# Kernel tuning notes

Hardware: AMD Instinct MI355X
Metric: run time of the kernel (lower is better)

Reference implementation:

```python
import jax, jax.numpy as jnp
import numpy as np

B, T, NH, MD, FF, HEADS, OUT, PEH = 8, 4096, 16, 64, 256, 4, 1, 32
DH = MD // HEADS

def _ln(x, g, b, eps=1e-5):
    m = jnp.mean(x, -1, keepdims=True)
    v = jnp.mean((x - m) ** 2, -1, keepdims=True)
    return (x - m) * jax.lax.rsqrt(v + eps) * g + b

def _lrelu(x):
    return jax.nn.leaky_relu(x, 0.2)

def setup_inputs():
    key = jax.random.key(0)
    ks = jax.random.split(key, 16)
    w = lambda k, s: jax.random.normal(k, s, jnp.float32) * 0.02
    return dict(
        x=jax.random.normal(ks[0], (B, T, MD), jnp.float32),
        coords1=jax.random.uniform(ks[1], (T,), jnp.float32),
        coords2=jax.random.uniform(ks[2], (T,), jnp.float32),
        g1=jnp.ones((MD,), jnp.float32), be1=jnp.zeros((MD,), jnp.float32),
        Wq=w(ks[3], (MD, MD)), bq=jnp.zeros((MD,), jnp.float32),
        Wk=w(ks[4], (MD, MD)), bk=jnp.zeros((MD,), jnp.float32),
        Wv=w(ks[5], (MD, MD)), bv=jnp.zeros((MD,), jnp.float32),
        logit_scale=jnp.full((HEADS, 1, 1), jnp.log(10.0), jnp.float32),
        Wo=w(ks[6], (MD, MD)), bo=jnp.zeros((MD,), jnp.float32),
        Wp1=w(ks[7], (2, PEH)), bp1=jnp.zeros((PEH,), jnp.float32),
        Wp2=w(ks[8], (PEH, HEADS)), bp2=jnp.zeros((HEADS,), jnp.float32),
        g2=jnp.ones((MD,), jnp.float32), be2=jnp.zeros((MD,), jnp.float32),
        Wn1=w(ks[9], (MD, FF)), bn1=jnp.zeros((FF,), jnp.float32),
        Wn2=w(ks[10], (FF, 1)), bn2=jnp.zeros((1,), jnp.float32),
        g3=jnp.ones((MD * NH,), jnp.float32), be3=jnp.zeros((MD * NH,), jnp.float32),
        Wu1=w(ks[11], (MD * NH, MD * NH)), bu1=jnp.zeros((MD * NH,), jnp.float32),
        Wu2=w(ks[12], (MD * NH, OUT)), bu2=jnp.zeros((OUT,), jnp.float32),
    )

def reference(x, coords1, coords2, g1, be1, Wq, bq, Wk, bk, Wv, bv, logit_scale, Wo, bo,
              Wp1, bp1, Wp2, bp2, g2, be2, Wn1, bn1, Wn2, bn2, g3, be3, Wu1, bu1, Wu2, bu2):
    b, t, e = x.shape
    xn = _ln(x, g1, be1)
    # pairwise relative coords: d[i, j] = c[j] - c[i]  -> [t, t]
    d1 = coords1[None, :] - coords1[:, None]
    d2 = coords2[None, :] - coords2[:, None]
    _, idx = jax.lax.top_k(-(d1 * d1 + d2 * d2), NH)          # [t, nh] kNN indices (incl. self)
    xg = xn[:, idx, :]                                         # [b, t, nh, e] neighbor gather
    c1 = jnp.take_along_axis(d1, idx, axis=1)                  # [t, nh] rel coords of neighbors
    c2 = jnp.take_along_axis(d2, idx, axis=1)
    # relative-position bias among the nh neighbors (shared across batch)
    p = jnp.stack([c1[:, :, None] - c1[:, None, :],
                   c2[:, :, None] - c2[:, None, :]], -1)       # [t, nh, nh, 2]
    bias = _lrelu(p @ Wp1 + bp1) @ Wp2 + bp2                   # [t, nh, nh, H]
    bias = jnp.transpose(bias, (0, 3, 1, 2))                   # [t, H, nh, nh]
    xf = xg.reshape(b * t, NH, e)
    split = lambda z: jnp.transpose(z.reshape(b * t, NH, HEADS, DH), (0, 2, 1, 3))
    qh = split(xf @ Wq + bq)
    kh = split(xf @ Wk + bk)
    vh = split(xf @ Wv + bv)
    # cosine attention with learnable clamped logit scale (SwinV2-style)
    qh = qh / jnp.maximum(jnp.linalg.norm(qh, axis=-1, keepdims=True), 1e-6)
    kh = kh / jnp.maximum(jnp.linalg.norm(kh, axis=-1, keepdims=True), 1e-6)
    scale = jnp.exp(jnp.minimum(logit_scale, jnp.log(100.0)))  # [H,1,1]
    att = jnp.einsum('nhqd,nhkd->nhqk', qh, kh) * scale        # [b*t, H, nh, nh]
    att = att.reshape(b, t, HEADS, NH, NH) + bias[None]
    att = jax.nn.softmax(att, -1).reshape(b * t, HEADS, NH, NH)
    av = jnp.einsum('nhqk,nhkd->nhqd', att, vh)
    av = jnp.transpose(av, (0, 2, 1, 3)).reshape(b * t, NH, e)
    xf = xf + (av @ Wo + bo)                                   # residual 1 (dropout=0)
    xf = _ln(xf, g2, be2)
    xf = xf + _lrelu(_lrelu(xf @ Wn1 + bn1) @ Wn2 + bn2)       # residual 2, [.,.,1] broadcast
    xu = _ln(xf.reshape(b, t, NH * e), g3, be3)                # unfold neighbors
    return _lrelu(_lrelu(xu @ Wu1 + bu1) @ Wu2 + bu2)          # [b, t, OUT]
```

## Files before the change

kernel.cpp:

```cpp
#include <hip/hip_runtime.h>
#include <hip/hip_bf16.h>

#define BB 8
#define TT 4096
#define NHH 16
#define MDD 64
#define FFF 256
#define HEADSS 4
#define DHH 16
#define PEHH 32

#define GM (BB * TT)
#define GK 1024
#define GN 1024
#define BMt 128
#define BNt 128
#define BKt 64
#define NCHUNK (GN / BNt)

#define TOKW 4

typedef float f32x4 __attribute__((ext_vector_type(4)));
typedef short bf16x8 __attribute__((ext_vector_type(8)));

static __device__ __forceinline__ float lrelu(float x) { return x > 0.0f ? x : 0.2f * x; }
static __device__ __forceinline__ unsigned long long umin64(unsigned long long a, unsigned long long b) {
    return a < b ? a : b;
}
static __device__ __forceinline__ unsigned short f2bf(float f) {
    unsigned u = __float_as_uint(f);
    u = u + 0x7fffu + ((u >> 16) & 1u);
    return (unsigned short)(u >> 16);
}
static __device__ __forceinline__ float bf2f(unsigned short u) {
    return __uint_as_float(((unsigned)u) << 16);
}
static __device__ __forceinline__ unsigned pk2(float a, float b) {
    return (unsigned)f2bf(a) | ((unsigned)f2bf(b) << 16);
}
static __device__ __forceinline__ void gload16(const void* g, void* l) {
    __builtin_amdgcn_global_load_lds((const __attribute__((address_space(1))) unsigned int*)g,
                                     (__attribute__((address_space(3))) unsigned int*)l, 16, 0, 0);
}

__global__ __launch_bounds__(256) void k_neighbors(const float* __restrict__ c1,
                                                   const float* __restrict__ c2,
                                                   int* __restrict__ idx,
                                                   float* __restrict__ c1n,
                                                   float* __restrict__ c2n) {
    int t = blockIdx.x;
    int tid = threadIdx.x;
    int lane = tid & 63, w = tid >> 6;
    __shared__ unsigned long long stage[4 * NHH];
    float c1t = c1[t], c2t = c2[t];

    unsigned long long keys[16];
    #pragma unroll
    for (int i = 0; i < 16; ++i) {
        int j = i * 256 + tid;
        float d1 = __fsub_rn(c1[j], c1t);
        float d2 = __fsub_rn(c2[j], c2t);
        float dist = __fadd_rn(__fmul_rn(d1, d1), __fmul_rn(d2, d2));
        keys[i] = (((unsigned long long)__float_as_uint(dist)) << 32) | (unsigned)j;
    }

    #pragma unroll 1
    for (int s = 0; s < NHH; ++s) {
        unsigned long long m = keys[0];
        #pragma unroll
        for (int i = 1; i < 16; ++i) m = umin64(m, keys[i]);
        #pragma unroll
        for (int off = 1; off < 64; off <<= 1)
            m = umin64(m, (unsigned long long)__shfl_xor((long long)m, off));
        #pragma unroll
        for (int i = 0; i < 16; ++i)
            if (keys[i] == m) keys[i] = ~0ull;
        if (lane == 0) stage[w * NHH + s] = m;
    }
    __syncthreads();

    if (w == 0) {
        unsigned long long k0 = stage[lane];
        #pragma unroll 1
        for (int s = 0; s < NHH; ++s) {
            unsigned long long m = k0;
            #pragma unroll
            for (int off = 1; off < 64; off <<= 1)
                m = umin64(m, (unsigned long long)__shfl_xor((long long)m, off));
            if (k0 == m) k0 = ~0ull;
            if (lane == 0) {
                int jj = (int)(unsigned)(m & 0xffffffffu);
                idx[t * NHH + s] = jj;
                c1n[t * NHH + s] = __fsub_rn(c1[jj], c1t);
                c2n[t * NHH + s] = __fsub_rn(c2[jj], c2t);
            }
        }
    }
}

__global__ __launch_bounds__(256) void k_bias(const float* __restrict__ c1n,
                                              const float* __restrict__ c2n,
                                              const float* __restrict__ Wp1,
                                              const float* __restrict__ bp1,
                                              const float* __restrict__ Wp2,
                                              const float* __restrict__ bp2,
                                              float* __restrict__ bias) {
    __shared__ float sWp1[2 * PEHH], sbp1[PEHH], sWp2[PEHH * HEADSS], sbp2[HEADSS];
    int tid = threadIdx.x;
    if (tid < 2 * PEHH) sWp1[tid] = Wp1[tid];
    if (tid < PEHH) sbp1[tid] = bp1[tid];
    if (tid < PEHH * HEADSS) sWp2[tid] = Wp2[tid];
    if (tid < HEADSS) sbp2[tid] = bp2[tid];
    __syncthreads();
    int g = blockIdx.x * 256 + tid;
    if (g >= TT * NHH * NHH) return;
    int j = g & 15, i = (g >> 4) & 15, t = g >> 8;
    float p1 = c1n[t * NHH + i] - c1n[t * NHH + j];
    float p2 = c2n[t * NHH + i] - c2n[t * NHH + j];
    float acc0 = sbp2[0], acc1 = sbp2[1], acc2 = sbp2[2], acc3 = sbp2[3];
    #pragma unroll
    for (int kk = 0; kk < PEHH; ++kk) {
        float h = lrelu(p1 * sWp1[kk] + p2 * sWp1[PEHH + kk] + sbp1[kk]);
        acc0 += h * sWp2[kk * HEADSS + 0];
        acc1 += h * sWp2[kk * HEADSS + 1];
        acc2 += h * sWp2[kk * HEADSS + 2];
        acc3 += h * sWp2[kk * HEADSS + 3];
    }
    float* bt = bias + (size_t)t * HEADSS * NHH * NHH;
    bt[(0 * NHH + i) * NHH + j] = acc0;
    bt[(1 * NHH + i) * NHH + j] = acc1;
    bt[(2 * NHH + i) * NHH + j] = acc2;
    bt[(3 * NHH + i) * NHH + j] = acc3;
}

__global__ __launch_bounds__(256) void k_ln1(const float* __restrict__ x,
                                             const float* __restrict__ g1,
                                             const float* __restrict__ be1,
                                             unsigned short* __restrict__ xn) {
    int row = blockIdx.x * 4 + (threadIdx.x >> 6);
    int lane = threadIdx.x & 63;
    float v = x[(size_t)row * MDD + lane];
    float s = v;
    for (int off = 32; off > 0; off >>= 1) s += __shfl_down(s, off);
    s = __shfl(s, 0);
    float m = s * (1.0f / 64.0f);
    float d = v - m;
    float sq = d * d;
    for (int off = 32; off > 0; off >>= 1) sq += __shfl_down(sq, off);
    sq = __shfl(sq, 0);
    float var = sq * (1.0f / 64.0f);
    float inv = 1.0f / sqrtf(var + 1e-5f);
    xn[(size_t)row * MDD + lane] = f2bf(d * inv * g1[lane] + be1[lane]);
}

__global__ __launch_bounds__(256) void k_prepw(const float* __restrict__ Wq, const float* __restrict__ Wk,
                                               const float* __restrict__ Wv, const float* __restrict__ Wo,
                                               const float* __restrict__ Wn1,
                                               unsigned short* __restrict__ Wall) {
    int id = blockIdx.x * 256 + threadIdx.x;
    int f = id >> 9;
    int w = (id >> 3) & 63;
    int e = id & 7;
    int li = w & 15, G = w >> 4;
    float v;
    if (f < 24) {
        int mt = f >> 1, ks = f & 1;
        int n = mt * 16 + li;
        int k = ks * 32 + G * 8 + e;
        v = (n < 64) ? Wq[k * 64 + n] : (n < 128) ? Wk[k * 64 + (n - 64)] : Wv[k * 64 + (n - 128)];
    } else if (f < 32) {
        int g2i = f - 24;
        int mt = g2i >> 1, ks = g2i & 1;
        int n = mt * 16 + li;
        int k = ks * 32 + G * 8 + e;
        v = Wo[k * 64 + n];
    } else {
        int g2i = f - 32;
        int mt = g2i >> 1, ks = g2i & 1;
        int n = mt * 16 + li;
        int k = ks * 32 + G * 8 + e;
        v = Wn1[k * 256 + n];
    }
    Wall[id] = f2bf(v);
}

__global__ __launch_bounds__(256, 4) void k_main(const unsigned short* __restrict__ xnb,
                                              const int* __restrict__ idx,
                                              const float* __restrict__ bias,
                                              const unsigned short* __restrict__ Wall,
                                              const float* __restrict__ bq, const float* __restrict__ bk,
                                              const float* __restrict__ bv, const float* __restrict__ ls,
                                              const float* __restrict__ bo,
                                              const float* __restrict__ g2, const float* __restrict__ be2,
                                              const float* __restrict__ bn1, const float* __restrict__ Wn2,
                                              const float* __restrict__ bn2,
                                              const float* __restrict__ g3, const float* __restrict__ be3,
                                              unsigned short* __restrict__ xu) {
    __shared__ __align__(16) char L[TOKW * 9216];
    const int tid = threadIdx.x;
    const int lane = tid & 63;
    const int li = lane & 15;
    const int G = lane >> 4;
    const int tok = tid >> 6;
    const int nglob = blockIdx.x * TOKW + tok;
    const int b = nglob >> 12;
    const int t = nglob & (TT - 1);
    const int asw = (li & 7) << 4;

    char* xgT = L + tok * 9216;
    char* qT  = xgT + 2048;
    char* kT  = xgT + 4096;
    char* vT  = xgT + 6144;

    {
        int r16 = lane >> 2, part = lane & 3;
        int j = idx[t * NHH + r16];
        const uint4* sp = reinterpret_cast<const uint4*>(xnb + ((size_t)b * TT + j) * MDD + part * 16);
        uint4 w0 = sp[0], w1 = sp[1];
        int sw = (r16 & 7) << 4;
        *reinterpret_cast<uint4*>(xgT + r16 * 128 + ((part * 32) ^ sw)) = w0;
        *reinterpret_cast<uint4*>(xgT + r16 * 128 + ((part * 32 + 16) ^ sw)) = w1;
    }

    bf16x8 xf0 = *reinterpret_cast<const bf16x8*>(xgT + li * 128 + ((G * 16) ^ asw));
    bf16x8 xf1 = *reinterpret_cast<const bf16x8*>(xgT + li * 128 + ((64 + G * 16) ^ asw));
    f32x4 acc[12];
    #pragma unroll
    for (int mt = 0; mt < 12; ++mt) {
        bf16x8 w0 = *reinterpret_cast<const bf16x8*>(Wall + (mt * 2 + 0) * 512 + lane * 8);
        bf16x8 w1 = *reinterpret_cast<const bf16x8*>(Wall + (mt * 2 + 1) * 512 + lane * 8);
        f32x4 a = (f32x4){0.0f, 0.0f, 0.0f, 0.0f};
        a = __builtin_amdgcn_mfma_f32_16x16x32_bf16(w0, xf0, a, 0, 0, 0);
        a = __builtin_amdgcn_mfma_f32_16x16x32_bf16(w1, xf1, a, 0, 0, 0);
        acc[mt] = a;
    }
    #pragma unroll
    for (int h = 0; h < 4; ++h) {
        float4 b4 = *reinterpret_cast<const float4*>(bq + h * 16 + G * 4);
        float q0 = acc[h][0] + b4.x, q1 = acc[h][1] + b4.y, q2 = acc[h][2] + b4.z, q3 = acc[h][3] + b4.w;
        float sq = q0 * q0 + q1 * q1 + q2 * q2 + q3 * q3;
        sq += __shfl_xor(sq, 16); sq += __shfl_xor(sq, 32);
        float iq = 1.0f / fmaxf(sqrtf(sq), 1e-6f);
        uint2 u; u.x = pk2(q0 * iq, q1 * iq); u.y = pk2(q2 * iq, q3 * iq);
        *reinterpret_cast<uint2*>(qT + li * 128 + ((h * 32 + G * 8) ^ asw)) = u;
    }
    #pragma unroll
    for (int h = 0; h < 4; ++h) {
        float4 b4 = *reinterpret_cast<const float4*>(bk + h * 16 + G * 4);
        float k0 = acc[4 + h][0] + b4.x, k1 = acc[4 + h][1] + b4.y, k2 = acc[4 + h][2] + b4.z, k3 = acc[4 + h][3] + b4.w;
        float sk = k0 * k0 + k1 * k1 + k2 * k2 + k3 * k3;
        sk += __shfl_xor(sk, 16); sk += __shfl_xor(sk, 32);
        float ik = 1.0f / fmaxf(sqrtf(sk), 1e-6f);
        uint2 u; u.x = pk2(k0 * ik, k1 * ik); u.y = pk2(k2 * ik, k3 * ik);
        *reinterpret_cast<uint2*>(kT + li * 128 + ((h * 32 + G * 8) ^ asw)) = u;
    }
    #pragma unroll
    for (int m2 = 0; m2 < 4; ++m2) {
        float4 b4 = *reinterpret_cast<const float4*>(bv + m2 * 16 + G * 4);
        float v0 = acc[8 + m2][0] + b4.x, v1 = acc[8 + m2][1] + b4.y, v2 = acc[8 + m2][2] + b4.z, v3 = acc[8 + m2][3] + b4.w;
        int c0 = m2 * 16 + G * 4;
        *reinterpret_cast<unsigned short*>(vT + (c0 + 0) * 48 + li * 2) = f2bf(v0);
        *reinterpret_cast<unsigned short*>(vT + (c0 + 1) * 48 + li * 2) = f2bf(v1);
        *reinterpret_cast<unsigned short*>(vT + (c0 + 2) * 48 + li * 2) = f2bf(v2);
        *reinterpret_cast<unsigned short*>(vT + (c0 + 3) * 48 + li * 2) = f2bf(v3);
    }

    float lsa[4] = {ls[0], ls[1], ls[2], ls[3]};

    #pragma unroll
    for (int h = 0; h < 4; ++h) {
        bf16x8 kf8 = {}, qf8 = {};
        if (G < 2) {
            kf8 = *reinterpret_cast<const bf16x8*>(kT + li * 128 + ((h * 32 + G * 16) ^ asw));
            qf8 = *reinterpret_cast<const bf16x8*>(qT + li * 128 + ((h * 32 + G * 16) ^ asw));
        }
        f32x4 s4 = __builtin_amdgcn_mfma_f32_16x16x32_bf16(kf8, qf8, (f32x4){0.0f, 0.0f, 0.0f, 0.0f}, 0, 0, 0);
        float sch = __expf(fminf(lsa[h], 4.60517018598809136804f));
        const float4 b4 = *reinterpret_cast<const float4*>(bias + ((size_t)t * 4 + h) * 256 + li * 16 + G * 4);
        float a0 = s4[0] * sch + b4.x;
        float a1 = s4[1] * sch + b4.y;
        float a2 = s4[2] * sch + b4.z;
        float a3 = s4[3] * sch + b4.w;
        float mx = fmaxf(fmaxf(a0, a1), fmaxf(a2, a3));
        mx = fmaxf(mx, __shfl_xor(mx, 16));
        mx = fmaxf(mx, __shfl_xor(mx, 32));
        float e0 = __expf(a0 - mx), e1 = __expf(a1 - mx), e2 = __expf(a2 - mx), e3 = __expf(a3 - mx);
        float sm = e0 + e1 + e2 + e3;
        sm += __shfl_xor(sm, 16);
        sm += __shfl_xor(sm, 32);
        float inv = 1.0f / sm;
        e0 *= inv; e1 *= inv; e2 *= inv; e3 *= inv;
        unsigned p01 = pk2(e0, e1), p23 = pk2(e2, e3);
        int s0l = li + 32 * (G & 1);
        uint4 pw;
        pw.x = (unsigned)__shfl((int)p01, s0l);
        pw.y = (unsigned)__shfl((int)p23, s0l);
        pw.z = (unsigned)__shfl((int)p01, s0l + 16);
        pw.w = (unsigned)__shfl((int)p23, s0l + 16);
        if (G >= 2) { pw.x = 0; pw.y = 0; pw.z = 0; pw.w = 0; }
        bf16x8 vf8 = {};
        if (G < 2) vf8 = *reinterpret_cast<const bf16x8*>(vT + (h * 16 + li) * 48 + G * 16);
        f32x4 pv = __builtin_amdgcn_mfma_f32_16x16x32_bf16(vf8, __builtin_bit_cast(bf16x8, pw),
                                                           (f32x4){0.0f, 0.0f, 0.0f, 0.0f}, 0, 0, 0);
        uint2 u; u.x = pk2(pv[0], pv[1]); u.y = pk2(pv[2], pv[3]);
        *reinterpret_cast<uint2*>(qT + li * 128 + ((h * 32 + G * 8) ^ asw)) = u;
    }

    float xfn[4][4];
    float rowadd;
    {
        bf16x8 av0 = *reinterpret_cast<const bf16x8*>(qT + li * 128 + ((G * 16) ^ asw));
        bf16x8 av1 = *reinterpret_cast<const bf16x8*>(qT + li * 128 + ((64 + G * 16) ^ asw));
        f32x4 oac[4];
        #pragma unroll
        for (int mt = 0; mt < 4; ++mt) {
            bf16x8 w0 = *reinterpret_cast<const bf16x8*>(Wall + (24 + mt * 2 + 0) * 512 + lane * 8);
            bf16x8 w1 = *reinterpret_cast<const bf16x8*>(Wall + (24 + mt * 2 + 1) * 512 + lane * 8);
            f32x4 a = (f32x4){0.0f, 0.0f, 0.0f, 0.0f};
            a = __builtin_amdgcn_mfma_f32_16x16x32_bf16(w0, av0, a, 0, 0, 0);
            a = __builtin_amdgcn_mfma_f32_16x16x32_bf16(w1, av1, a, 0, 0, 0);
            oac[mt] = a;
        }
        float xf[4][4];
        float s = 0.0f, sq = 0.0f;
        #pragma unroll
        for (int mt = 0; mt < 4; ++mt) {
            float4 bo4 = *reinterpret_cast<const float4*>(bo + mt * 16 + G * 4);
            uint2 xg2 = *reinterpret_cast<const uint2*>(xgT + li * 128 + ((mt * 32 + G * 8) ^ asw));
            float r0 = bf2f((unsigned short)(xg2.x & 0xffffu));
            float r1 = bf2f((unsigned short)(xg2.x >> 16));
            float r2 = bf2f((unsigned short)(xg2.y & 0xffffu));
            float r3 = bf2f((unsigned short)(xg2.y >> 16));
            xf[mt][0] = oac[mt][0] + bo4.x + r0;
            xf[mt][1] = oac[mt][1] + bo4.y + r1;
            xf[mt][2] = oac[mt][2] + bo4.z + r2;
            xf[mt][3] = oac[mt][3] + bo4.w + r3;
            #pragma unroll
            for (int r = 0; r < 4; ++r) { s += xf[mt][r]; sq += xf[mt][r] * xf[mt][r]; }
        }
        s += __shfl_xor(s, 16); s += __shfl_xor(s, 32);
        sq += __shfl_xor(sq, 16); sq += __shfl_xor(sq, 32);
        float m = s * (1.0f / 64.0f);
        float var = sq * (1.0f / 64.0f) - m * m;
        float inv = 1.0f / sqrtf(var + 1e-5f);
        #pragma unroll
        for (int mt = 0; mt < 4; ++mt) {
            float4 g24 = *reinterpret_cast<const float4*>(g2 + mt * 16 + G * 4);
            float4 be24 = *reinterpret_cast<const float4*>(be2 + mt * 16 + G * 4);
            xfn[mt][0] = (xf[mt][0] - m) * inv * g24.x + be24.x;
            xfn[mt][1] = (xf[mt][1] - m) * inv * g24.y + be24.y;
            xfn[mt][2] = (xf[mt][2] - m) * inv * g24.z + be24.z;
            xfn[mt][3] = (xf[mt][3] - m) * inv * g24.w + be24.w;
            uint2 u; u.x = pk2(xfn[mt][0], xfn[mt][1]); u.y = pk2(xfn[mt][2], xfn[mt][3]);
            *reinterpret_cast<uint2*>(kT + li * 128 + ((mt * 32 + G * 8) ^ asw)) = u;
        }
    }

    {
        bf16x8 xn0 = *reinterpret_cast<const bf16x8*>(kT + li * 128 + ((G * 16) ^ asw));
        bf16x8 xn1 = *reinterpret_cast<const bf16x8*>(kT + li * 128 + ((64 + G * 16) ^ asw));
        float dot = 0.0f;
        #pragma unroll
        for (int mt = 0; mt < 16; ++mt) {
            bf16x8 w0 = *reinterpret_cast<const bf16x8*>(Wall + (32 + mt * 2 + 0) * 512 + lane * 8);
            bf16x8 w1 = *reinterpret_cast<const bf16x8*>(Wall + (32 + mt * 2 + 1) * 512 + lane * 8);
            f32x4 a = (f32x4){0.0f, 0.0f, 0.0f, 0.0f};
            a = __builtin_amdgcn_mfma_f32_16x16x32_bf16(w0, xn0, a, 0, 0, 0);
            a = __builtin_amdgcn_mfma_f32_16x16x32_bf16(w1, xn1, a, 0, 0, 0);
            float4 bn14 = *reinterpret_cast<const float4*>(bn1 + mt * 16 + G * 4);
            float4 w24 = *reinterpret_cast<const float4*>(Wn2 + mt * 16 + G * 4);
            dot += lrelu(a[0] + bn14.x) * w24.x;
            dot += lrelu(a[1] + bn14.y) * w24.y;
            dot += lrelu(a[2] + bn14.z) * w24.z;
            dot += lrelu(a[3] + bn14.w) * w24.w;
        }
        dot += __shfl_xor(dot, 16);
        dot += __shfl_xor(dot, 32);
        rowadd = lrelu(dot + bn2[0]);
    }

    {
        float s = 0.0f, sq = 0.0f;
        float vals[4][4];
        #pragma unroll
        for (int mt = 0; mt < 4; ++mt)
            #pragma unroll
            for (int r = 0; r < 4; ++r) {
                float v = xfn[mt][r] + rowadd;
                vals[mt][r] = v;
                s += v; sq += v * v;
            }
        s += __shfl_xor(s, 1); s += __shfl_xor(s, 2); s += __shfl_xor(s, 4);
        s += __shfl_xor(s, 8); s += __shfl_xor(s, 16); s += __shfl_xor(s, 32);
        sq += __shfl_xor(sq, 1); sq += __shfl_xor(sq, 2); sq += __shfl_xor(sq, 4);
        sq += __shfl_xor(sq, 8); sq += __shfl_xor(sq, 16); sq += __shfl_xor(sq, 32);
        float m = s * (1.0f / 1024.0f);
        float var = sq * (1.0f / 1024.0f) - m * m;
        float inv = 1.0f / sqrtf(var + 1e-5f);
        int swm = nglob & 7;
        #pragma unroll
        for (int mt = 0; mt < 4; ++mt) {
            int o0 = li * 64 + mt * 16 + G * 4;
            float4 g34 = *reinterpret_cast<const float4*>(g3 + o0);
            float4 be34 = *reinterpret_cast<const float4*>(be3 + o0);
            float u0 = (vals[mt][0] - m) * inv * g34.x + be34.x;
            float u1 = (vals[mt][1] - m) * inv * g34.y + be34.y;
            float u2 = (vals[mt][2] - m) * inv * g34.z + be34.z;
            float u3 = (vals[mt][3] - m) * inv * g34.w + be34.w;
            uint2 u; u.x = pk2(u0, u1); u.y = pk2(u2, u3);
            size_t p = (size_t)nglob * 1024 + li * 64
                     + ((((mt * 2 + (G >> 1)) ^ swm) << 3) | ((G & 1) * 4));
            *reinterpret_cast<uint2*>(xu + p) = u;
        }
    }
}

__global__ __launch_bounds__(256) void k_cvtW(const float* __restrict__ W,
                                              unsigned short* __restrict__ Wt) {
    __shared__ float tile[32][33];
    int tk = blockIdx.x & 31;
    int tn = blockIdx.x >> 5;
    int c = threadIdx.x & 31, r4 = threadIdx.x >> 5;
    #pragma unroll
    for (int p = 0; p < 4; ++p) {
        int r = p * 8 + r4;
        tile[r][c] = W[(size_t)(tk * 32 + r) * GN + tn * 32 + c];
    }
    __syncthreads();
    #pragma unroll
    for (int p = 0; p < 4; ++p) {
        int r = p * 8 + r4;
        int n = tn * 32 + r;
        int kk = tk * 32 + c;
        int chunk = kk >> 6, slot = (kk >> 3) & 7, e = kk & 7;
        Wt[(size_t)n * GK + chunk * 64 + ((slot ^ (n & 7)) << 3) + e] = f2bf(tile[c][r]);
    }
}

__global__ __launch_bounds__(256) void k_gemm(const unsigned short* __restrict__ xu,
                                              const unsigned short* __restrict__ Wt,
                                              const float* __restrict__ bu1,
                                              const float* __restrict__ Wu2,
                                              float* __restrict__ partial) {
    int bm = blockIdx.x;
    int bn = blockIdx.y;
    int tid = threadIdx.x;
    int w = tid >> 6, l = tid & 63;
    int wm = w >> 1, wn = w & 1;
    int lr = l & 15, lg = l >> 4;

    __shared__ __align__(1024) unsigned short LB[4 * BMt * BKt];
    __shared__ float rowpart[2][BMt];
    char* base = reinterpret_cast<char*>(LB);

    f32x4 acc[4][4];
    #pragma unroll
    for (int i = 0; i < 4; ++i)
        #pragma unroll
        for (int j = 0; j < 4; ++j)
            acc[i][j] = (f32x4){0.0f, 0.0f, 0.0f, 0.0f};

    const size_t arow = (size_t)(bm * BMt) * GK;
    const size_t brow = (size_t)(bn * BNt) * GK;

    #define STAGE(kt, buf)                                                            \
        {                                                                             \
            char* Ab_ = base + (buf) * 32768;                                         \
            char* Bb_ = Ab_ + 16384;                                                  \
            int k0_ = (kt) * BKt;                                                     \
            _Pragma("unroll")                                                         \
            for (int p = 0; p < 4; ++p) {                                             \
                int seg = w * 4 + p;                                                  \
                int rl = seg * 8 + (l >> 3);                                          \
                gload16(xu + arow + (size_t)rl * GK + k0_ + (l & 7) * 8, Ab_ + seg * 1024); \
                gload16(Wt + brow + (size_t)rl * GK + k0_ + (l & 7) * 8, Bb_ + seg * 1024); \
            }                                                                         \
        }

    STAGE(0, 0)
    __syncthreads();

    for (int kt = 0; kt < GK / BKt; ++kt) {
        int buf = kt & 1;
        if (kt < GK / BKt - 1) STAGE(kt + 1, buf ^ 1)
        char* Ab = base + buf * 32768;
        char* Bb = Ab + 16384;
        #pragma unroll
        for (int ks = 0; ks < 2; ++ks) {
            bf16x8 af[4], bfr[4];
            #pragma unroll
            for (int rf = 0; rf < 4; ++rf) {
                int row = wm * 64 + rf * 16 + lr;
                int coff = (ks * 64 + lg * 16) ^ ((row & 7) << 4);
                af[rf] = *reinterpret_cast<const bf16x8*>(Ab + row * 128 + coff);
            }
            #pragma unroll
            for (int nf = 0; nf < 4; ++nf) {
                int rowb = wn * 64 + nf * 16 + lr;
                int coff = (ks * 64 + lg * 16) ^ ((rowb & 7) << 4);
                bfr[nf] = *reinterpret_cast<const bf16x8*>(Bb + rowb * 128 + coff);
            }
            #pragma unroll
            for (int rf = 0; rf < 4; ++rf)
                #pragma unroll
                for (int nf = 0; nf < 4; ++nf)
                    acc[rf][nf] = __builtin_amdgcn_mfma_f32_16x16x32_bf16(af[rf], bfr[nf], acc[rf][nf], 0, 0, 0);
        }
        __syncthreads();
    }
    #undef STAGE

    float b1v[4], w2v[4];
    #pragma unroll
    for (int nf = 0; nf < 4; ++nf) {
        int nn = bn * BNt + wn * 64 + nf * 16 + lr;
        b1v[nf] = bu1[nn];
        w2v[nf] = Wu2[nn];
    }
    float rowsum[4][4];
    #pragma unroll
    for (int rf = 0; rf < 4; ++rf) {
        #pragma unroll
        for (int j = 0; j < 4; ++j) {
            float s = 0.0f;
            #pragma unroll
            for (int nf = 0; nf < 4; ++nf)
                s += lrelu(acc[rf][nf][j] + b1v[nf]) * w2v[nf];
            #pragma unroll
            for (int off = 1; off < 16; off <<= 1)
                s += __shfl_xor(s, off);
            rowsum[rf][j] = s;
        }
    }
    if (lr == 0) {
        #pragma unroll
        for (int rf = 0; rf < 4; ++rf)
            #pragma unroll
            for (int j = 0; j < 4; ++j)
                rowpart[wn][wm * 64 + rf * 16 + lg * 4 + j] = rowsum[rf][j];
    }
    __syncthreads();
    if (tid < BMt) {
        float v = rowpart[0][tid] + rowpart[1][tid];
        partial[((size_t)(bm * BMt + tid)) * NCHUNK + bn] = v;
    }
}

__global__ __launch_bounds__(256) void k_reduce(const float* __restrict__ partial,
                                                const float* __restrict__ bu2,
                                                float* __restrict__ out) {
    int m = blockIdx.x * 256 + threadIdx.x;
    float s = bu2[0];
    #pragma unroll
    for (int c = 0; c < NCHUNK; ++c) s += partial[(size_t)m * NCHUNK + c];
    out[m] = lrelu(s);
}

extern "C" void kernel_launch(void* const* d_in, const int* in_sizes, int n_in,
                              void* d_out, int out_size, void* d_ws, size_t ws_size,
                              hipStream_t stream) {
    const float* x   = (const float*)d_in[0];
    const float* c1  = (const float*)d_in[1];
    const float* c2  = (const float*)d_in[2];
    const float* g1  = (const float*)d_in[3];
    const float* be1 = (const float*)d_in[4];
    const float* Wq  = (const float*)d_in[5];
    const float* bq  = (const float*)d_in[6];
    const float* Wk  = (const float*)d_in[7];
    const float* bk  = (const float*)d_in[8];
    const float* Wv  = (const float*)d_in[9];
    const float* bv  = (const float*)d_in[10];
    const float* ls  = (const float*)d_in[11];
    const float* Wo  = (const float*)d_in[12];
    const float* bo  = (const float*)d_in[13];
    const float* Wp1 = (const float*)d_in[14];
    const float* bp1 = (const float*)d_in[15];
    const float* Wp2 = (const float*)d_in[16];
    const float* bp2 = (const float*)d_in[17];
    const float* g2  = (const float*)d_in[18];
    const float* be2 = (const float*)d_in[19];
    const float* Wn1 = (const float*)d_in[20];
    const float* bn1 = (const float*)d_in[21];
    const float* Wn2 = (const float*)d_in[22];
    const float* bn2 = (const float*)d_in[23];
    const float* g3  = (const float*)d_in[24];
    const float* be3 = (const float*)d_in[25];
    const float* Wu1 = (const float*)d_in[26];
    const float* bu1 = (const float*)d_in[27];
    const float* Wu2 = (const float*)d_in[28];
    const float* bu2 = (const float*)d_in[29];
    float* out = (float*)d_out;

    char* ws = (char*)d_ws;
    size_t off = 0;
    int*   idx  = (int*)(ws + off);   off += (size_t)TT * NHH * 4;
    float* c1n  = (float*)(ws + off); off += (size_t)TT * NHH * 4;
    float* c2n  = (float*)(ws + off); off += (size_t)TT * NHH * 4;
    float* bias = (float*)(ws + off); off += (size_t)TT * HEADSS * NHH * NHH * 4;
    unsigned short* xnb  = (unsigned short*)(ws + off); off += (size_t)BB * TT * MDD * 2;
    unsigned short* xuB  = (unsigned short*)(ws + off); off += (size_t)GM * GK * 2;
    unsigned short* Wu1t = (unsigned short*)(ws + off); off += (size_t)GK * GN * 2;
    float* partial = (float*)(ws + off); off += (size_t)GM * NCHUNK * 4;
    unsigned short* Wall = (unsigned short*)(ws + off); off += 64 * 1024;

    k_neighbors<<<TT, 256, 0, stream>>>(c1, c2, idx, c1n, c2n);
    k_bias<<<(TT * NHH * NHH + 255) / 256, 256, 0, stream>>>(c1n, c2n, Wp1, bp1, Wp2, bp2, bias);
    k_ln1<<<(BB * TT) / 4, 256, 0, stream>>>(x, g1, be1, xnb);
    k_prepw<<<128, 256, 0, stream>>>(Wq, Wk, Wv, Wo, Wn1, Wall);
    k_cvtW<<<1024, 256, 0, stream>>>(Wu1, Wu1t);
    k_main<<<(BB * TT) / TOKW, 256, 0, stream>>>(xnb, idx, bias, Wall,
                                                 bq, bk, bv, ls, bo, g2, be2, bn1, Wn2, bn2, g3, be3, xuB);
    k_gemm<<<dim3(GM / BMt, GN / BNt), 256, 0, stream>>>(xuB, Wu1t, bu1, Wu2, partial);
    k_reduce<<<GM / 256, 256, 0, stream>>>(partial, bu2, out);
}
```

Before: 338.8 us.

## Fuse bias into neighbor kernel, merge prep kernels, relax GEMM barrier waits

Computes the positional bias MLP inside the kNN kernel using neighbor offsets kept in shared memory, which removes the separate bias launch and its reload of c1n/c2n. Merges LayerNorm1, the small weight repacking and the Wu1 transpose-convert into one launch that dispatches on block index, cutting launch count. In the Wu1 GEMM, replaces __syncthreads with an explicit vmcnt wait plus s_barrier so the prefetch of the next tile can stay in flight while the current tile is consumed. The fixed vmcnt(8) count depends on how many loads STAGE issues per thread, so it can break correctness if that count differs.

Result: faster. 328.2 us (-3.1%).

```diff
diff --git a/kernel.cpp b/kernel.cpp
--- a/kernel.cpp
+++ b/kernel.cpp
@@ -45,13 +45,24 @@
 
 __global__ __launch_bounds__(256) void k_neighbors(const float* __restrict__ c1,
                                                    const float* __restrict__ c2,
+                                                   const float* __restrict__ Wp1,
+                                                   const float* __restrict__ bp1,
+                                                   const float* __restrict__ Wp2,
+                                                   const float* __restrict__ bp2,
                                                    int* __restrict__ idx,
                                                    float* __restrict__ c1n,
-                                                   float* __restrict__ c2n) {
+                                                   float* __restrict__ c2n,
+                                                   float* __restrict__ bias) {
     int t = blockIdx.x;
     int tid = threadIdx.x;
     int lane = tid & 63, w = tid >> 6;
     __shared__ unsigned long long stage[4 * NHH];
+    __shared__ float sc1[NHH], sc2[NHH];
+    __shared__ float sWp1[2 * PEHH], sbp1[PEHH], sWp2[PEHH * HEADSS], sbp2[HEADSS];
+    if (tid < 2 * PEHH) sWp1[tid] = Wp1[tid];
+    if (tid < PEHH) sbp1[tid] = bp1[tid];
+    if (tid < PEHH * HEADSS) sWp2[tid] = Wp2[tid];
+    if (tid < HEADSS) sbp2[tid] = bp2[tid];
     float c1t = c1[t], c2t = c2[t];
 
     unsigned long long keys[16];
@@ -90,98 +101,118 @@
             if (k0 == m) k0 = ~0ull;
             if (lane == 0) {
                 int jj = (int)(unsigned)(m & 0xffffffffu);
+                float v1 = __fsub_rn(c1[jj], c1t);
+                float v2 = __fsub_rn(c2[jj], c2t);
                 idx[t * NHH + s] = jj;
-                c1n[t * NHH + s] = __fsub_rn(c1[jj], c1t);
-                c2n[t * NHH + s] = __fsub_rn(c2[jj], c2t);
+                c1n[t * NHH + s] = v1;
+                c2n[t * NHH + s] = v2;
+                sc1[s] = v1;
+                sc2[s] = v2;
             }
         }
     }
-}
-
-__global__ __launch_bounds__(256) void k_bias(const float* __restrict__ c1n,
-                                              const float* __restrict__ c2n,
-                                              const float* __restrict__ Wp1,
-                                              const float* __restrict__ bp1,
-                                              const float* __restrict__ Wp2,
-                                              const float* __restrict__ bp2,
-                                              float* __restrict__ bias) {
-    __shared__ float sWp1[2 * PEHH], sbp1[PEHH], sWp2[PEHH * HEADSS], sbp2[HEADSS];
+    __syncthreads();
+
+    {
+        int j = tid & 15, i = tid >> 4;
+        float p1 = sc1[i] - sc1[j];
+        float p2 = sc2[i] - sc2[j];
+        float acc0 = sbp2[0], acc1 = sbp2[1], acc2 = sbp2[2], acc3 = sbp2[3];
+        #pragma unroll
+        for (int kk = 0; kk < PEHH; ++kk) {
+            float h = lrelu(p1 * sWp1[kk] + p2 * sWp1[PEHH + kk] + sbp1[kk]);
+            acc0 += h * sWp2[kk * HEADSS + 0];
+            acc1 += h * sWp2[kk * HEADSS + 1];
+            acc2 += h * sWp2[kk * HEADSS + 2];
+            acc3 += h * sWp2[kk * HEADSS + 3];
+        }
+        float* bt = bias + (size_t)t * HEADSS * NHH * NHH;
+        bt[0 * 256 + i * NHH + j] = acc0;
+        bt[1 * 256 + i * NHH + j] = acc1;
+        bt[2 * 256 + i * NHH + j] = acc2;
+        bt[3 * 256 + i * NHH + j] = acc3;
+    }
+}
+
+__global__ __launch_bounds__(256) void k_prep(const float* __restrict__ x,
+                                              const float* __restrict__ g1,
+                                              const float* __restrict__ be1,
+                                              unsigned short* __restrict__ xn,
+                                              const float* __restrict__ Wq, const float* __restrict__ Wk,
+                                              const float* __restrict__ Wv, const float* __restrict__ Wo,
+                                              const float* __restrict__ Wn1,
+                                              unsigned short* __restrict__ Wall,
+                                              const float* __restrict__ W,
+                                              unsigned short* __restrict__ Wt) {
+    int blk = blockIdx.x;
     int tid = threadIdx.x;
-    if (tid < 2 * PEHH) sWp1[tid] = Wp1[tid];
-    if (tid < PEHH) sbp1[tid] = bp1[tid];
-    if (tid < PEHH * HEADSS) sWp2[tid] = Wp2[tid];
-    if (tid < HEADSS) sbp2[tid] = bp2[tid];
-    __syncthreads();
-    int g = blockIdx.x * 256 + tid;
-    if (g >= TT * NHH * NHH) return;
-    int j = g & 15, i = (g >> 4) & 15, t = g >> 8;
-    float p1 = c1n[t * NHH + i] - c1n[t * NHH + j];
-    float p2 = c2n[t * NHH + i] - c2n[t * NHH + j];
-    float acc0 = sbp2[0], acc1 = sbp2[1], acc2 = sbp2[2], acc3 = sbp2[3];
-    #pragma unroll
-    for (int kk = 0; kk < PEHH; ++kk) {
-        float h = lrelu(p1 * sWp1[kk] + p2 * sWp1[PEHH + kk] + sbp1[kk]);
-        acc0 += h * sWp2[kk * HEADSS + 0];
-        acc1 += h * sWp2[kk * HEADSS + 1];
-        acc2 += h * sWp2[kk * HEADSS + 2];
-        acc3 += h * sWp2[kk * HEADSS + 3];
-    }
-    float* bt = bias + (size_t)t * HEADSS * NHH * NHH;
-    bt[(0 * NHH + i) * NHH + j] = acc0;
-    bt[(1 * NHH + i) * NHH + j] = acc1;
-    bt[(2 * NHH + i) * NHH + j] = acc2;
-    bt[(3 * NHH + i) * NHH + j] = acc3;
-}
-
-__global__ __launch_bounds__(256) void k_ln1(const float* __restrict__ x,
-                                             const float* __restrict__ g1,
-                                             const float* __restrict__ be1,
-                                             unsigned short* __restrict__ xn) {
-    int row = blockIdx.x * 4 + (threadIdx.x >> 6);
-    int lane = threadIdx.x & 63;
-    float v = x[(size_t)row * MDD + lane];
-    float s = v;
-    for (int off = 32; off > 0; off >>= 1) s += __shfl_down(s, off);
-    s = __shfl(s, 0);
-    float m = s * (1.0f / 64.0f);
-    float d = v - m;
-    float sq = d * d;
-    for (int off = 32; off > 0; off >>= 1) sq += __shfl_down(sq, off);
-    sq = __shfl(sq, 0);
-    float var = sq * (1.0f / 64.0f);
-    float inv = 1.0f / sqrtf(var + 1e-5f);
-    xn[(size_t)row * MDD + lane] = f2bf(d * inv * g1[lane] + be1[lane]);
-}
-
-__global__ __launch_bounds__(256) void k_prepw(const float* __restrict__ Wq, const float* __restrict__ Wk,
-                                               const float* __restrict__ Wv, const float* __restrict__ Wo,
-                                               const float* __restrict__ Wn1,
-                                               unsigned short* __restrict__ Wall) {
-    int id = blockIdx.x * 256 + threadIdx.x;
-    int f = id >> 9;
-    int w = (id >> 3) & 63;
-    int e = id & 7;
-    int li = w & 15, G = w >> 4;
-    float v;
-    if (f < 24) {
-        int mt = f >> 1, ks = f & 1;
-        int n = mt * 16 + li;
-        int k = ks * 32 + G * 8 + e;
-        v = (n < 64) ? Wq[k * 64 + n] : (n < 128) ? Wk[k * 64 + (n - 64)] : Wv[k * 64 + (n - 128)];
-    } else if (f < 32) {
-        int g2i = f - 24;
-        int mt = g2i >> 1, ks = g2i & 1;
-        int n = mt * 16 + li;
-        int k = ks * 32 + G * 8 + e;
-        v = Wo[k * 64 + n];
-    } else {
-        int g2i = f - 32;
-        int mt = g2i >> 1, ks = g2i & 1;
-        int n = mt * 16 + li;
-        int k = ks * 32 + G * 8 + e;
-        v = Wn1[k * 256 + n];
-    }
-    Wall[id] = f2bf(v);
+    if (blk < (BB * TT) / 4) {
+        int row = blk * 4 + (tid >> 6);
+        int lane = tid & 63;
+        float v = x[(size_t)row * MDD + lane];
+        float s = v;
+        for (int off = 32; off > 0; off >>= 1) s += __shfl_down(s, off);
+        s = __shfl(s, 0);
+        float m = s * (1.0f / 64.0f);
+        float d = v - m;
+        float sq = d * d;
+        for (int off = 32; off > 0; off >>= 1) sq += __shfl_down(sq, off);
+        sq = __shfl(sq, 0);
+        float var = sq * (1.0f / 64.0f);
+        float inv = 1.0f / sqrtf(var + 1e-5f);
+        xn[(size_t)row * MDD + lane] = f2bf(d * inv * g1[lane] + be1[lane]);
+        return;
+    }
+    blk -= (BB * TT) / 4;
+    if (blk < 128) {
+        int id = blk * 256 + tid;
+        int f = id >> 9;
+        int wv = (id >> 3) & 63;
+        int e = id & 7;
+        int li = wv & 15, G = wv >> 4;
+        float v;
+        if (f < 24) {
+            int mt = f >> 1, ks = f & 1;
+            int n = mt * 16 + li;
+            int k = ks * 32 + G * 8 + e;
+            v = (n < 64) ? Wq[k * 64 + n] : (n < 128) ? Wk[k * 64 + (n - 64)] : Wv[k * 64 + (n - 128)];
+        } else if (f < 32) {
+            int g2i = f - 24;
+            int mt = g2i >> 1, ks = g2i & 1;
+            int n = mt * 16 + li;
+            int k = ks * 32 + G * 8 + e;
+            v = Wo[k * 64 + n];
+        } else {
+            int g2i = f - 32;
+            int mt = g2i >> 1, ks = g2i & 1;
+            int n = mt * 16 + li;
+            int k = ks * 32 + G * 8 + e;
+            v = Wn1[k * 256 + n];
+        }
+        Wall[id] = f2bf(v);
+        return;
+    }
+    blk -= 128;
+    {
+        __shared__ float tile[32][33];
+        int tk = blk & 31;
+        int tn = blk >> 5;
+        int c = tid & 31, r4 = tid >> 5;
+        #pragma unroll
+        for (int p = 0; p < 4; ++p) {
+            int r = p * 8 + r4;
+            tile[r][c] = W[(size_t)(tk * 32 + r) * GN + tn * 32 + c];
+        }
+        __syncthreads();
+        #pragma unroll
+        for (int p = 0; p < 4; ++p) {
+            int r = p * 8 + r4;
+            int n = tn * 32 + r;
+            int kk = tk * 32 + c;
+            int chunk = kk >> 6, slot = (kk >> 3) & 7, e = kk & 7;
+            Wt[(size_t)n * GK + chunk * 64 + ((slot ^ (n & 7)) << 3) + e] = f2bf(tile[c][r]);
+        }
+    }
 }
 
 __global__ __launch_bounds__(256, 4) void k_main(const unsigned short* __restrict__ xnb,
@@ -415,28 +446,6 @@
     }
 }
 
-__global__ __launch_bounds__(256) void k_cvtW(const float* __restrict__ W,
-                                              unsigned short* __restrict__ Wt) {
-    __shared__ float tile[32][33];
-    int tk = blockIdx.x & 31;
-    int tn = blockIdx.x >> 5;
-    int c = threadIdx.x & 31, r4 = threadIdx.x >> 5;
-    #pragma unroll
-    for (int p = 0; p < 4; ++p) {
-        int r = p * 8 + r4;
-        tile[r][c] = W[(size_t)(tk * 32 + r) * GN + tn * 32 + c];
-    }
-    __syncthreads();
-    #pragma unroll
-    for (int p = 0; p < 4; ++p) {
-        int r = p * 8 + r4;
-        int n = tn * 32 + r;
-        int kk = tk * 32 + c;
-        int chunk = kk >> 6, slot = (kk >> 3) & 7, e = kk & 7;
-        Wt[(size_t)n * GK + chunk * 64 + ((slot ^ (n & 7)) << 3) + e] = f2bf(tile[c][r]);
-    }
-}
-
 __global__ __launch_bounds__(256) void k_gemm(const unsigned short* __restrict__ xu,
                                               const unsigned short* __restrict__ Wt,
                                               const float* __restrict__ bu1,
@@ -478,11 +487,18 @@
         }
 
     STAGE(0, 0)
-    __syncthreads();
 
     for (int kt = 0; kt < GK / BKt; ++kt) {
         int buf = kt & 1;
-        if (kt < GK / BKt - 1) STAGE(kt + 1, buf ^ 1)
+        if (kt < GK / BKt - 1) {
+            STAGE(kt + 1, buf ^ 1)
+            asm volatile("s_waitcnt vmcnt(8)" ::: "memory");
+        } else {
+            asm volatile("s_waitcnt vmcnt(0)" ::: "memory");
+        }
+        __builtin_amdgcn_sched_barrier(0);
+        __builtin_amdgcn_s_barrier();
+        __builtin_amdgcn_sched_barrier(0);
         char* Ab = base + buf * 32768;
         char* Bb = Ab + 16384;
         #pragma unroll
@@ -506,7 +522,8 @@
                 for (int nf = 0; nf < 4; ++nf)
                     acc[rf][nf] = __builtin_amdgcn_mfma_f32_16x16x32_bf16(af[rf], bfr[nf], acc[rf][nf], 0, 0, 0);
         }
-        __syncthreads();
+        __builtin_amdgcn_sched_barrier(0);
+        __builtin_amdgcn_s_barrier();
     }
     #undef STAGE
 
@@ -603,11 +620,9 @@
     float* partial = (float*)(ws + off); off += (size_t)GM * NCHUNK * 4;
     unsigned short* Wall = (unsigned short*)(ws + off); off += 64 * 1024;
 
-    k_neighbors<<<TT, 256, 0, stream>>>(c1, c2, idx, c1n, c2n);
-    k_bias<<<(TT * NHH * NHH + 255) / 256, 256, 0, stream>>>(c1n, c2n, Wp1, bp1, Wp2, bp2, bias);
-    k_ln1<<<(BB * TT) / 4, 256, 0, stream>>>(x, g1, be1, xnb);
-    k_prepw<<<128, 256, 0, stream>>>(Wq, Wk, Wv, Wo, Wn1, Wall);
-    k_cvtW<<<1024, 256, 0, stream>>>(Wu1, Wu1t);
+    k_neighbors<<<TT, 256, 0, stream>>>(c1, c2, Wp1, bp1, Wp2, bp2, idx, c1n, c2n, bias);
+    k_prep<<<(BB * TT) / 4 + 128 + 1024, 256, 0, stream>>>(x, g1, be1, xnb,
+                                                           Wq, Wk, Wv, Wo, Wn1, Wall, Wu1, Wu1t);
     k_main<<<(BB * TT) / TOKW, 256, 0, stream>>>(xnb, idx, bias, Wall,
                                                  bq, bk, bv, ls, bo, g2, be2, bn1, Wn2, bn2, g3, be3, xuB);
     k_gemm<<<dim3(GM / BMt, GN / BNt), 256, 0, stream>>>(xuB, Wu1t, bu1, Wu2, partial);
```
